# Kernel optimization log

Measured on AMD Instinct MI355X. Metric: run time of the kernel, lower is better.

## Reference

```python
import jax, jax.numpy as jnp
import numpy as np

B, S, D, H, DFF = 8, 1024, 1024, 16, 4096
DK = D // H
NEG = -1000000000.0


def layernorm(x, g, b, eps=1e-5):
    mu = jnp.mean(x, axis=-1, keepdims=True)
    var = jnp.mean((x - mu) ** 2, axis=-1, keepdims=True)
    return (x - mu) / jnp.sqrt(var + eps) * g + b


def setup_inputs() -> dict:
    key = jax.random.key(0)
    ks = jax.random.split(key, 16)
    s = 0.02
    inp = {
        "x": jax.random.normal(ks[0], (B, S, D), jnp.float32),
        "binary_mask": jax.random.randint(ks[1], (B, S), 0, 2, jnp.int32),
        # per-head projections stacked: [H, D, DK]
        "Wq": jax.random.normal(ks[2], (H, D, DK), jnp.float32) * s,
        "bq": jnp.zeros((H, DK), jnp.float32),
        "Wk": jax.random.normal(ks[3], (H, D, DK), jnp.float32) * s,
        "bk": jnp.zeros((H, DK), jnp.float32),
        "Wv": jax.random.normal(ks[4], (H, D, DK), jnp.float32) * s,
        "bv": jnp.zeros((H, DK), jnp.float32),
        "Wo": jax.random.normal(ks[5], (D, D), jnp.float32) * s,
        "bo": jnp.zeros((D,), jnp.float32),
        "ga": jnp.ones((D,), jnp.float32),
        "ba": jnp.zeros((D,), jnp.float32),
        "W1": jax.random.normal(ks[6], (D, DFF), jnp.float32) * s,
        "b1": jnp.zeros((DFF,), jnp.float32),
        "W2": jax.random.normal(ks[7], (DFF, D), jnp.float32) * s,
        "b2": jnp.zeros((D,), jnp.float32),
        "gf": jnp.ones((D,), jnp.float32),
        "bf": jnp.zeros((D,), jnp.float32),
    }
    return inp


def encoder_fwd(x, binary_mask, Wq, bq, Wk, bk, Wv, bv, Wo, bo, ga, ba, W1, b1, W2, b2, gf, bf):
    # --- multi-head self-attention (heads vectorized over h axis) ---
    q = jnp.einsum("bsd,hdk->bhsk", x, Wq) + bq[None, :, None, :]
    k = jnp.einsum("bsd,hdk->bhsk", x, Wk) + bk[None, :, None, :]
    v = jnp.einsum("bsd,hdk->bhsk", x, Wv) + bv[None, :, None, :]
    score = jnp.einsum("bhik,bhjk->bhij", q, k) / jnp.sqrt(jnp.float32(DK))
    # mask: binary_mask is over KEY positions, broadcast over query dim
    score = score + jnp.where(binary_mask[:, None, None, :] == 0, NEG, 0.0)
    # NOTE: original code softmaxes over dim=1 of [B,Sq,Sk] -> the QUERY axis
    probs = jax.nn.softmax(score, axis=2)
    ctx = jnp.einsum("bhij,bhjk->bhik", probs, v)  # [B,H,S,DK]
    ctx = jnp.transpose(ctx, (0, 2, 1, 3)).reshape(x.shape[0], x.shape[1], D)
    attn_out = ctx @ Wo + bo
    y = layernorm(x + attn_out, ga, ba)
    # --- FFN ---
    h = jax.nn.relu(y @ W1 + b1)
    ffn_out = h @ W2 + b2
    return layernorm(y + ffn_out, gf, bf)


def reference(x, binary_mask, Wq, bq, Wk, bk, Wv, bv, Wo, bo, ga, ba, W1, b1, W2, b2, gf, bf):
    return encoder_fwd(x, binary_mask, Wq, bq, Wk, bk, Wv, bv, Wo, bo, ga, ba, W1, b1, W2, b2, gf, bf)
```

## Files before the change

kernel.cpp:

```cpp
#include <hip/hip_runtime.h>
#include <hip/hip_bf16.h>

typedef __bf16 bf16;
typedef __bf16 bf16x8 __attribute__((ext_vector_type(8)));
typedef __bf16 bf16x4 __attribute__((ext_vector_type(4)));
typedef float  f32x4  __attribute__((ext_vector_type(4)));

#define NB 8
#define NS 1024
#define ND 1024
#define NH 16
#define NDK 64
#define NDFF 4096

static __device__ __forceinline__ f32x4 mfma16(bf16x8 a, bf16x8 b, f32x4 c) {
    return __builtin_amdgcn_mfma_f32_16x16x32_bf16(a, b, c, 0, 0, 0);
}

#define GLDS(g, l) __builtin_amdgcn_global_load_lds( \
    (const __attribute__((address_space(1))) void*)(g), \
    (__attribute__((address_space(3))) void*)(l), 16, 0, 0)

__global__ __launch_bounds__(256) void cvt_x(const float* __restrict__ in,
                                             bf16* __restrict__ out, int n4)
{
    int idx = blockIdx.x * 256 + threadIdx.x;
    if (idx >= n4) return;
    float4 v = ((const float4*)in)[idx];
    bf16x4 o = { (bf16)v.x, (bf16)v.y, (bf16)v.z, (bf16)v.w };
    ((bf16x4*)out)[idx] = o;
}

__global__ __launch_bounds__(256) void prep_transpose(
    const float* __restrict__ Wq, const float* __restrict__ Wk, const float* __restrict__ Wv,
    const float* __restrict__ Wo, const float* __restrict__ W1, const float* __restrict__ W2,
    bf16* __restrict__ wqkvT, bf16* __restrict__ WoT,
    bf16* __restrict__ W1T, bf16* __restrict__ W2T)
{
    __shared__ float T[64][65];
    int bid = blockIdx.x;
    const float* src; bf16* dst; int srcLd, dstLd, tR, tC; bool scale = false;
    if (bid < 768) {
        int mat = bid >> 4, ty = bid & 15;
        int h = mat & 15, type = mat >> 4;
        const float* W = (type == 0) ? Wq : (type == 1 ? Wk : Wv);
        src = W + (size_t)h * ND * NDK;
        srcLd = NDK; tR = ty * 64; tC = 0;
        dst = wqkvT + ((size_t)type * 1024 + h * 64) * ND;
        dstLd = ND;
        scale = (type == 0);
    } else if (bid < 1024) {
        int b2 = bid - 768; int ty = b2 >> 4, tx = b2 & 15;
        src = Wo; srcLd = ND; tR = ty * 64; tC = tx * 64; dst = WoT; dstLd = ND;
    } else if (bid < 2048) {
        int b2 = bid - 1024; int ty = b2 >> 6, tx = b2 & 63;
        src = W1; srcLd = NDFF; tR = ty * 64; tC = tx * 64; dst = W1T; dstLd = ND;
    } else {
        int b2 = bid - 2048; int ty = b2 >> 4, tx = b2 & 15;
        src = W2; srcLd = ND; tR = ty * 64; tC = tx * 64; dst = W2T; dstLd = NDFF;
    }
    int t = threadIdx.x;
    int c0 = t & 63, r0 = t >> 6;
    #pragma unroll
    for (int rr = 0; rr < 16; rr++) {
        int row = rr * 4 + r0;
        T[row][c0] = src[(size_t)(tR + row) * srcLd + tC + c0];
    }
    __syncthreads();
    #pragma unroll
    for (int cc = 0; cc < 16; cc++) {
        int col = cc * 4 + r0;
        float v = T[c0][col];
        if (scale) v *= 0.125f;
        dst[(size_t)(tC + col) * dstLd + tR + c0] = (bf16)v;
    }
}

__global__ void prep_bias(const float* __restrict__ bq, const float* __restrict__ bk,
                          const float* __restrict__ bv, float* __restrict__ bqkv)
{
    int n = blockIdx.x * 256 + threadIdx.x;
    if (n >= 3072) return;
    int type = n >> 10, hk = n & 1023;
    const float* bb = (type == 0) ? bq : (type == 1 ? bk : bv);
    float v = bb[hk];
    if (type == 0) v *= 0.125f;
    bqkv[n] = v;
}

__global__ __launch_bounds__(256) void mask_scan(const int* __restrict__ mask,
                                                 int* __restrict__ newpos,
                                                 int* __restrict__ Ucnt)
{
    int b = blockIdx.x, t = threadIdx.x;
    __shared__ int sums[256];
    __shared__ int scans[257];
    const int* mb = mask + b * NS;
    int m[4], s = 0;
    #pragma unroll
    for (int k = 0; k < 4; k++) { m[k] = (mb[t * 4 + k] != 0) ? 1 : 0; s += m[k]; }
    sums[t] = s;
    __syncthreads();
    if (t == 0) {
        int acc = 0;
        for (int i = 0; i < 256; i++) { scans[i] = acc; acc += sums[i]; }
        scans[256] = acc;
        Ucnt[b] = acc;
    }
    __syncthreads();
    int U = scans[256];
    int p = scans[t];
    #pragma unroll
    for (int k = 0; k < 4; k++) {
        int j = t * 4 + k;
        newpos[b * NS + j] = m[k] ? p : U + (j - p);
        p += m[k];
    }
}

__global__ __launch_bounds__(256) void cvec_kernel(const bf16* __restrict__ Vb,
                                                   const int* __restrict__ Ucnt,
                                                   float* __restrict__ cvec)
{
    int bh = blockIdx.x, b = bh >> 4;
    int U = Ucnt[b];
    int t = threadIdx.x, kk = t & 63, ss = t >> 6;
    const bf16* Vp = Vb + (size_t)bh * NS * NDK;
    float a = 0.f;
    for (int s = U + ss; s < NS; s += 4) a += (float)Vp[s * NDK + kk];
    __shared__ float red[4][64];
    red[ss][kk] = a;
    __syncthreads();
    if (ss == 0)
        cvec[bh * 64 + kk] = (red[0][kk] + red[1][kk] + red[2][kk] + red[3][kk]) * (1.f / 1024.f);
}

__device__ __forceinline__ void gemm_bt_core(
    const bf16* __restrict__ A, const bf16* __restrict__ BT, int K,
    int rowBase, int colBase, f32x4 (&acc)[4][4], bf16* As, bf16* Bs)
{
    const int tid = threadIdx.x;
    const int lane = tid & 63, wid = tid >> 6;
    const int wr = (wid >> 1) * 64, wc = (wid & 1) * 64;
    const int lrow = lane & 15, lq = lane >> 4;
    const int srow = wid * 32 + (lane >> 3);
    const int gblk = (lane & 7) ^ ((lane >> 3) & 7);
    const bf16* Arow = A + (size_t)(rowBase + srow) * K + gblk * 8;
    const bf16* Brow = BT + (size_t)(colBase + srow) * K + gblk * 8;
    const int co0 = ((lq) ^ (lrow & 7)) * 8;
    const int co1 = ((4 + lq) ^ (lrow & 7)) * 8;
    f32x4 zz = {0.f, 0.f, 0.f, 0.f};
    #pragma unroll
    for (int i = 0; i < 4; i++)
        #pragma unroll
        for (int j = 0; j < 4; j++) acc[i][j] = zz;
    for (int k0 = 0; k0 < K; k0 += 64) {
        __syncthreads();
        #pragma unroll
        for (int it = 0; it < 4; it++)
            GLDS(Arow + (size_t)it * 8 * K + k0, As + (wid * 32 + it * 8) * 64);
        #pragma unroll
        for (int it = 0; it < 4; it++)
            GLDS(Brow + (size_t)it * 8 * K + k0, Bs + (wid * 32 + it * 8) * 64);
        __syncthreads();
        #pragma unroll
        for (int kh = 0; kh < 2; kh++) {
            const int co = kh ? co1 : co0;
            bf16x8 af[4], bfr[4];
            #pragma unroll
            for (int tt = 0; tt < 4; tt++) {
                af[tt]  = *(const bf16x8*)&As[(wr + tt * 16 + lrow) * 64 + co];
                bfr[tt] = *(const bf16x8*)&Bs[(wc + tt * 16 + lrow) * 64 + co];
            }
            #pragma unroll
            for (int i = 0; i < 4; i++)
                #pragma unroll
                for (int j = 0; j < 4; j++)
                    acc[i][j] = mfma16(af[i], bfr[j], acc[i][j]);
        }
    }
}

__device__ __forceinline__ void gemm8p(
    const bf16* __restrict__ A, const bf16* __restrict__ BT, int K,
    int rowBase, int colBase, f32x4 (&acc)[8][4], bf16* As, bf16* Bs)
{
    constexpr int SETSZ = 256 * 64;
    const int tid = threadIdx.x, lane = tid & 63, wid = tid >> 6;
    const int wm = wid >> 2, wn = wid & 3;
    const int lrow = lane & 15, lq = lane >> 4;
    const int s8 = lane >> 3, gblk = (lane & 7) ^ s8;
    const int co0 = (lq ^ (lrow & 7)) * 8;
    const int co1 = ((4 + lq) ^ (lrow & 7)) * 8;
    f32x4 zz = {0.f, 0.f, 0.f, 0.f};
    #pragma unroll
    for (int i = 0; i < 8; i++)
        #pragma unroll
        for (int j = 0; j < 4; j++) acc[i][j] = zz;
    const bf16* Ag = A  + (size_t)(rowBase + wid * 8 + s8) * K + gblk * 8;
    const bf16* Bg = BT + (size_t)(colBase + wid * 8 + s8) * K + gblk * 8;

#define SG_A(kt, set, h) do { \
    GLDS(Ag + (size_t)((h) * 128) * K + (kt) * 64, \
         As + (set) * SETSZ + ((h) * 128 + wid * 8) * 64); \
    GLDS(Ag + (size_t)((h) * 128 + 64) * K + (kt) * 64, \
         As + (set) * SETSZ + ((h) * 128 + 64 + wid * 8) * 64); \
} while (0)
#define SG_B(kt, set, h) do { \
    GLDS(Bg + (size_t)((h) * 128) * K + (kt) * 64, \
         Bs + (set) * SETSZ + ((h) * 128 + wid * 8) * 64); \
    GLDS(Bg + (size_t)((h) * 128 + 64) * K + (kt) * 64, \
         Bs + (set) * SETSZ + ((h) * 128 + 64 + wid * 8) * 64); \
} while (0)
#define RD_A(dst, base, ms) do { _Pragma("unroll") for (int i_ = 0; i_ < 4; i_++) { \
    int ro_ = (wm * 128 + (ms) * 64 + i_ * 16 + lrow) * 64; \
    dst[i_][0] = *(const bf16x8*)&(base)[ro_ + co0]; \
    dst[i_][1] = *(const bf16x8*)&(base)[ro_ + co1]; } } while (0)
#define RD_B(dst, base, ns) do { _Pragma("unroll") for (int j_ = 0; j_ < 2; j_++) { \
    int ro_ = (wn * 64 + (ns) * 32 + j_ * 16 + lrow) * 64; \
    dst[j_][0] = *(const bf16x8*)&(base)[ro_ + co0]; \
    dst[j_][1] = *(const bf16x8*)&(base)[ro_ + co1]; } } while (0)
#define CL8(av, bv, ms, ns) do { \
    __builtin_amdgcn_s_setprio(1); \
    _Pragma("unroll") for (int i_ = 0; i_ < 4; i_++) \
    _Pragma("unroll") for (int j_ = 0; j_ < 2; j_++) { \
        acc[(ms) * 4 + i_][(ns) * 2 + j_] = \
            mfma16(av[i_][0], bv[j_][0], acc[(ms) * 4 + i_][(ns) * 2 + j_]); \
        acc[(ms) * 4 + i_][(ns) * 2 + j_] = \
            mfma16(av[i_][1], bv[j_][1], acc[(ms) * 4 + i_][(ns) * 2 + j_]); } \
    __builtin_amdgcn_s_setprio(0); \
} while (0)
#define BAR8 __builtin_amdgcn_s_barrier()
#define VM4 asm volatile("s_waitcnt vmcnt(4)" ::: "memory")
#define VM0 asm volatile("s_waitcnt vmcnt(0)" ::: "memory")

    const int nt = K >> 6, nIter = nt >> 1;
    SG_B(0, 0, 0); SG_B(0, 0, 1);
    SG_A(0, 0, 0); SG_A(0, 0, 1);
    SG_B(1, 1, 0); SG_B(1, 1, 1);
    VM4; BAR8;
    const bf16* A0b = As;           const bf16* B0b = Bs;
    const bf16* A1b = As + SETSZ;   const bf16* B1b = Bs + SETSZ;
    for (int J = 0; J < nIter; ++J) {
        const int v = 2 * J + 1;
        const bool pf = (J + 1 < nIter);
        bf16x8 a0[4][2], a1[4][2], b0[2][2], b1[2][2];
        RD_A(a0, A0b, 0); RD_B(b0, B0b, 0);
        SG_A(v, 1, 0);
        BAR8; CL8(a0, b0, 0, 0); BAR8;
        RD_B(b1, B0b, 1);
        SG_A(v, 1, 1);
        BAR8; CL8(a0, b1, 0, 1); BAR8;
        RD_A(a1, A0b, 1);
        if (pf) SG_B(v + 1, 0, 0);
        BAR8; CL8(a1, b1, 1, 1); BAR8;
        if (pf) SG_B(v + 1, 0, 1);
        BAR8; CL8(a1, b0, 1, 0);
        if (pf) { VM4; } else { VM0; }
        BAR8;
        RD_A(a0, A1b, 0); RD_B(b0, B1b, 0);
        if (pf) SG_A(v + 1, 0, 0);
        BAR8; CL8(a0, b0, 0, 0); BAR8;
        RD_B(b1, B1b, 1);
        if (pf) SG_A(v + 1, 0, 1);
        BAR8; CL8(a0, b1, 0, 1); BAR8;
        RD_A(a1, A1b, 1);
        if (pf) SG_B(v + 2, 1, 0);
        BAR8; CL8(a1, b1, 1, 1); BAR8;
        if (pf) SG_B(v + 2, 1, 1);
        BAR8; CL8(a1, b0, 1, 0);
        if (pf) { VM4; } else { VM0; }
        BAR8;
    }
#undef SG_A
#undef SG_B
#undef RD_A
#undef RD_B
#undef CL8
#undef BAR8
#undef VM4
#undef VM0
}

__device__ __forceinline__ void gemmB_core(
    const bf16* __restrict__ A, const bf16* __restrict__ BT, int K,
    int rowBase, int colBase, f32x4 (&acc)[4][4], bf16* As, bf16* Bs)
{
    constexpr int ABUF = 128 * 64, BBUF = 256 * 64;
    const int tid = threadIdx.x, lane = tid & 63, wid = tid >> 6;
    const int wm = wid >> 2, wn = wid & 3;
    const int lrow = lane & 15, lq = lane >> 4;
    const int srow = lane >> 3, gblk = (lane & 7) ^ srow;
    const int co0 = (lq ^ (lrow & 7)) * 8;
    const int co1 = ((4 + lq) ^ (lrow & 7)) * 8;
    f32x4 zz = {0.f, 0.f, 0.f, 0.f};
    #pragma unroll
    for (int i = 0; i < 4; i++)
        #pragma unroll
        for (int j = 0; j < 4; j++) acc[i][j] = zz;
    const bf16* Ag = A  + (size_t)(rowBase + wid * 8 + srow) * K + gblk * 8;
    const bf16* Bg = BT + (size_t)(colBase + wid * 8 + srow) * K + gblk * 8;

#define SGA2(kt, bi, rr) GLDS(Ag + (size_t)(kt) * 64 + (size_t)(rr) * 64 * K, \
                              As + (bi) * ABUF + ((rr) * 64 + wid * 8) * 64)
#define SGB2(kt, bi, rr) GLDS(Bg + (size_t)(kt) * 64 + (size_t)(rr) * 64 * K, \
                              Bs + (bi) * BBUF + ((rr) * 64 + wid * 8) * 64)
#define RDA2() do { _Pragma("unroll") for (int i_ = 0; i_ < 4; i_++) { \
    int ro_ = (wm * 64 + i_ * 16 + lrow) * 64; \
    af[i_][0] = *(const bf16x8*)&Ab[ro_ + co0]; \
    af[i_][1] = *(const bf16x8*)&Ab[ro_ + co1]; } } while (0)
#define RDB2(dst, NS_) do { _Pragma("unroll") for (int j_ = 0; j_ < 2; j_++) { \
    int ro_ = (wn * 64 + (NS_) * 32 + j_ * 16 + lrow) * 64; \
    dst[j_][0] = *(const bf16x8*)&Bb[ro_ + co0]; \
    dst[j_][1] = *(const bf16x8*)&Bb[ro_ + co1]; } } while (0)
#define CLUSTER_B(bfx, JO) do { \
    __builtin_amdgcn_s_barrier(); \
    asm volatile("s_waitcnt lgkmcnt(0)" ::: "memory"); \
    __builtin_amdgcn_sched_barrier(0); \
    __builtin_amdgcn_s_setprio(1); \
    _Pragma("unroll") \
    for (int i_ = 0; i_ < 4; i_++) \
        _Pragma("unroll") \
        for (int j_ = 0; j_ < 2; j_++) { \
            acc[i_][(JO) + j_] = mfma16(af[i_][0], bfx[j_][0], acc[i_][(JO) + j_]); \
            acc[i_][(JO) + j_] = mfma16(af[i_][1], bfx[j_][1], acc[i_][(JO) + j_]); \
        } \
    __builtin_amdgcn_s_setprio(0); \
} while (0)

    const int nt = K >> 6;
    SGA2(0, 0, 0); SGA2(0, 0, 1);
    SGB2(0, 0, 0); SGB2(0, 0, 1); SGB2(0, 0, 2); SGB2(0, 0, 3);
    SGA2(1, 1, 0); SGA2(1, 1, 1);
    SGB2(1, 1, 0); SGB2(1, 1, 1); SGB2(1, 1, 2); SGB2(1, 1, 3);
    asm volatile("s_waitcnt vmcnt(6)" ::: "memory");
    __builtin_amdgcn_s_barrier();

    int ci = 0, si = 2;
    for (int t = 0; t < nt; ++t) {
        const bf16* Ab = As + ci * ABUF;
        const bf16* Bb = Bs + ci * BBUF;
        const bool pf = (t + 2 < nt);
        bf16x8 af[4][2], bf0[2][2], bf1[2][2];
        RDA2(); RDB2(bf0, 0);
        if (pf) { SGA2(t + 2, si, 0); SGA2(t + 2, si, 1); SGB2(t + 2, si, 0); SGB2(t + 2, si, 1); }
        CLUSTER_B(bf0, 0);
        __builtin_amdgcn_s_barrier();
        RDB2(bf1, 1);
        if (pf) { SGB2(t + 2, si, 2); SGB2(t + 2, si, 3); }
        CLUSTER_B(bf1, 2);
        if (pf)                asm volatile("s_waitcnt vmcnt(6)" ::: "memory");
        else if (t + 1 < nt)   asm volatile("s_waitcnt vmcnt(0)" ::: "memory");
        __builtin_amdgcn_s_barrier();
        ci = (ci == 2) ? 0 : ci + 1;
        si = (si == 2) ? 0 : si + 1;
    }
#undef SGA2
#undef SGB2
#undef RDA2
#undef RDB2
#undef CLUSTER_B
}

__global__ __launch_bounds__(256) void g1_qkv(
    const bf16* __restrict__ x, const bf16* __restrict__ wqkvT, const float* __restrict__ bqkv,
    const int* __restrict__ newpos,
    bf16* __restrict__ Q, bf16* __restrict__ Kb, bf16* __restrict__ Vb)
{
    __shared__ bf16 As[128 * 64], Bs[128 * 64];
    f32x4 acc[4][4];
    int rowBase = blockIdx.x * 128, colBase = blockIdx.y * 128;
    gemm_bt_core(x, wqkvT, ND, rowBase, colBase, acc, As, Bs);
    const int tid = threadIdx.x, lane = tid & 63, wid = tid >> 6;
    const int wr = (wid >> 1) * 64, wc = (wid & 1) * 64, lrow = lane & 15, lq = lane >> 4;
    const int type = colBase >> 10;
    int spv[4][4];
    if (type != 0) {
        #pragma unroll
        for (int i = 0; i < 4; i++)
            #pragma unroll
            for (int r = 0; r < 4; r++) {
                int grow = rowBase + wr + i * 16 + lq * 4 + r;
                spv[i][r] = newpos[grow];
            }
    }
    #pragma unroll
    for (int j = 0; j < 4; j++) {
        int gcol = colBase + wc + j * 16 + lrow;
        float bias = bqkv[gcol];
        int h = (gcol >> 6) & 15, kk = gcol & 63;
        bf16* dst = (type == 0) ? Q : (type == 1 ? Kb : Vb);
        #pragma unroll
        for (int i = 0; i < 4; i++) {
            #pragma unroll
            for (int r = 0; r < 4; r++) {
                int grow = rowBase + wr + i * 16 + lq * 4 + r;
                int b = grow >> 10;
                int s = (type == 0) ? (grow & 1023) : spv[i][r];
                dst[((size_t)(b * NH + h) * NS + s) * NDK + kk] = (bf16)(acc[i][j][r] + bias);
            }
        }
    }
}

__global__ __launch_bounds__(256) void vt_trans(
    const bf16* __restrict__ Vb, bf16* __restrict__ Vt)
{
    __shared__ bf16 T[64 * 72];
    int bh = blockIdx.y, s0 = blockIdx.x * 64;
    const bf16* src = Vb + ((size_t)bh * NS + s0) * NDK;
    int tid = threadIdx.x;
    #pragma unroll
    for (int it = 0; it < 2; it++) {
        int g = tid + it * 256;
        int row = g >> 3, c = (g & 7) * 8;
        *(bf16x8*)&T[row * 72 + c] = *(const bf16x8*)&src[row * NDK + c];
    }
    __syncthreads();
    #pragma unroll
    for (int it = 0; it < 2; it++) {
        int g = tid + it * 256;
        int kk = g >> 3, sc = (g & 7) * 8;
        bf16x8 v;
        #pragma unroll
        for (int t = 0; t < 8; t++) v[t] = T[(sc + t) * 72 + kk];
        *(bf16x8*)&Vt[((size_t)bh * NDK + kk) * NS + s0 + sc] = v;
    }
}

__global__ __launch_bounds__(256) void g2_stats(
    const bf16* __restrict__ Q, const bf16* __restrict__ Kb,
    const int* __restrict__ Ucnt, float2* __restrict__ alpha)
{
    __shared__ bf16 Qs[128 * 64];
    int bh = blockIdx.y, b = bh >> 4;
    int jBase = blockIdx.x * 128;
    int U = Ucnt[b];
    const int tid = threadIdx.x;
    if (jBase >= U) {
        if (tid < 128) {
            float2 z; z.x = 0.f; z.y = 0.f;
            alpha[(size_t)bh * NS + jBase + tid] = z;
        }
        return;
    }
    const bf16* Kp = Kb + (size_t)bh * NS * NDK;
    const bf16* Qp = Q + (size_t)bh * NS * NDK;
    const int lane = tid & 63, wid = tid >> 6;
    const int lrow = lane & 15, lq = lane >> 4;
    bf16x8 kf[2][2];
    #pragma unroll
    for (int jt = 0; jt < 2; jt++)
        #pragma unroll
        for (int kh = 0; kh < 2; kh++)
            kf[jt][kh] = *(const bf16x8*)&Kp[(size_t)(jBase + wid * 32 + jt * 16 + lrow) * NDK + kh * 32 + lq * 8];
    const int srow = lane >> 3;
    const int gblk = (lane & 7) ^ srow;
    float Lacc[2][4];
    #pragma unroll
    for (int jt = 0; jt < 2; jt++)
        #pragma unroll
        for (int r = 0; r < 4; r++) Lacc[jt][r] = 0.f;
    f32x4 zz = {0.f, 0.f, 0.f, 0.f};
    for (int i0 = 0; i0 < NS; i0 += 128) {
        __syncthreads();
        #pragma unroll
        for (int it = 0; it < 4; it++)
            GLDS(Qp + (size_t)(i0 + wid * 32 + it * 8 + srow) * NDK + gblk * 8,
                 Qs + (wid * 32 + it * 8) * 64);
        __syncthreads();
        #pragma unroll
        for (int it = 0; it < 8; it++) {
            bf16x8 qb[2];
            #pragma unroll
            for (int kh = 0; kh < 2; kh++)
                qb[kh] = *(const bf16x8*)&Qs[(it * 16 + lrow) * 64 + ((kh * 4 + lq) ^ (lrow & 7)) * 8];
            #pragma unroll
            for (int jt = 0; jt < 2; jt++) {
                f32x4 s = mfma16(kf[jt][0], qb[0], zz);
                s = mfma16(kf[jt][1], qb[1], s);
                #pragma unroll
                for (int r = 0; r < 4; r++) Lacc[jt][r] += __expf(s[r]);
            }
        }
    }
    #pragma unroll
    for (int jt = 0; jt < 2; jt++) {
        #pragma unroll
        for (int r = 0; r < 4; r++) {
            float v = Lacc[jt][r];
            v += __shfl_xor(v, 1); v += __shfl_xor(v, 2);
            v += __shfl_xor(v, 4); v += __shfl_xor(v, 8);
            if (lrow == 0) {
                int j = jBase + wid * 32 + jt * 16 + lq * 4 + r;
                float2 ac;
                ac.x = (j < U) ? 1.f / v : 0.f;
                ac.y = 0.f;
                alpha[(size_t)bh * NS + j] = ac;
            }
        }
    }
}

__global__ __launch_bounds__(256) void g3_ctx(
    const bf16* __restrict__ Q, const bf16* __restrict__ Kb, const bf16* __restrict__ Vt,
    const float2* __restrict__ alpha, const int* __restrict__ Ucnt,
    const float* __restrict__ cvec, bf16* __restrict__ ctx)
{
    __shared__ bf16 Ks[64 * 64];
    __shared__ bf16 Vs[64 * 64];
    __shared__ bf16 Ps[4 * 64 * 64];
    int bh = blockIdx.y, iBase = blockIdx.x * 256;
    int b = bh >> 4, h = bh & 15;
    int U = Ucnt[b];
    int Ur = (U + 63) & ~63;
    const bf16* Qp = Q + (size_t)bh * NS * NDK;
    const bf16* Kp = Kb + (size_t)bh * NS * NDK;
    const bf16* Vp = Vt + (size_t)bh * NDK * NS;
    const float2* al = alpha + (size_t)bh * NS;
    const int tid = threadIdx.x, lane = tid & 63, wid = tid >> 6;
    const int lrow = lane & 15, lq = lane >> 4;
    const int iw = iBase + wid * 64;
    bf16x8 qf[4][2];
    #pragma unroll
    for (int it = 0; it < 4; it++)
        #pragma unroll
        for (int kh = 0; kh < 2; kh++)
            qf[it][kh] = *(const bf16x8*)&Qp[(size_t)(iw + it * 16 + lrow) * NDK + kh * 32 + lq * 8];
    const int srow = lane >> 3;
    const int gblk = (lane & 7) ^ srow;
    f32x4 cacc[4][4];
    f32x4 zz = {0.f, 0.f, 0.f, 0.f};
    #pragma unroll
    for (int it = 0; it < 4; it++)
        #pragma unroll
        for (int kt = 0; kt < 4; kt++) cacc[it][kt] = zz;
    bf16* Pw = Ps + wid * 64 * 64;
    for (int j0 = 0; j0 < Ur; j0 += 64) {
        __syncthreads();
        #pragma unroll
        for (int it = 0; it < 2; it++)
            GLDS(Kp + (size_t)(j0 + wid * 16 + it * 8 + srow) * NDK + gblk * 8,
                 Ks + (wid * 16 + it * 8) * 64);
        #pragma unroll
        for (int it = 0; it < 2; it++)
            GLDS(Vp + (size_t)(wid * 16 + it * 8 + srow) * NS + j0 + gblk * 8,
                 Vs + (wid * 16 + it * 8) * 64);
        __syncthreads();
        bf16x8 kb[4][2];
        #pragma unroll
        for (int jt = 0; jt < 4; jt++)
            #pragma unroll
            for (int kh = 0; kh < 2; kh++)
                kb[jt][kh] = *(const bf16x8*)&Ks[(jt * 16 + lrow) * 64 + ((kh * 4 + lq) ^ (lrow & 7)) * 8];
        #pragma unroll
        for (int jt = 0; jt < 4; jt++) {
            float2 acj[4];
            #pragma unroll
            for (int r = 0; r < 4; r++) acj[r] = al[j0 + jt * 16 + lq * 4 + r];
            #pragma unroll
            for (int it = 0; it < 4; it++) {
                f32x4 s = mfma16(kb[jt][0], qf[it][0], zz);
                s = mfma16(kb[jt][1], qf[it][1], s);
                bf16x4 pv;
                #pragma unroll
                for (int r = 0; r < 4; r++)
                    pv[r] = (bf16)(acj[r].x * __expf(s[r]) + acj[r].y);
                int i = it * 16 + lrow;
                int jb = jt * 2 + (lq >> 1);
                *(bf16x4*)&Pw[i * 64 + ((jb ^ (i & 7)) * 8) + (lq & 1) * 4] = pv;
            }
        }
        bf16x8 vb[4][2];
        #pragma unroll
        for (int kt = 0; kt < 4; kt++)
            #pragma unroll
            for (int kh = 0; kh < 2; kh++)
                vb[kt][kh] = *(const bf16x8*)&Vs[(kt * 16 + lrow) * 64 + ((kh * 4 + lq) ^ (lrow & 7)) * 8];
        #pragma unroll
        for (int it = 0; it < 4; it++) {
            bf16x8 pa[2];
            #pragma unroll
            for (int kh = 0; kh < 2; kh++)
                pa[kh] = *(const bf16x8*)&Pw[(it * 16 + lrow) * 64 + ((kh * 4 + lq) ^ (lrow & 7)) * 8];
            #pragma unroll
            for (int kt = 0; kt < 4; kt++) {
                cacc[it][kt] = mfma16(pa[0], vb[kt][0], cacc[it][kt]);
                cacc[it][kt] = mfma16(pa[1], vb[kt][1], cacc[it][kt]);
            }
        }
    }
    #pragma unroll
    for (int kt = 0; kt < 4; kt++) {
        int col = h * NDK + kt * 16 + lrow;
        float cv = cvec[bh * 64 + kt * 16 + lrow];
        #pragma unroll
        for (int it = 0; it < 4; it++) {
            #pragma unroll
            for (int r = 0; r < 4; r++) {
                int i = iw + it * 16 + lq * 4 + r;
                ctx[(size_t)(b * NS + i) * ND + col] = (bf16)(cacc[it][kt][r] + cv);
            }
        }
    }
}

__global__ __launch_bounds__(256) void g4_proj(
    const bf16* __restrict__ ctx, const bf16* __restrict__ WoT, const float* __restrict__ bo,
    const bf16* __restrict__ xb, bf16* __restrict__ t1b)
{
    __shared__ bf16 As[128 * 64], Bs[128 * 64];
    f32x4 acc[4][4];
    int rowBase = blockIdx.x * 128, colBase = blockIdx.y * 128;
    gemm_bt_core(ctx, WoT, ND, rowBase, colBase, acc, As, Bs);
    const int tid = threadIdx.x, lane = tid & 63, wid = tid >> 6;
    const int wr = (wid >> 1) * 64, wc = (wid & 1) * 64, lrow = lane & 15, lq = lane >> 4;
    #pragma unroll
    for (int j = 0; j < 4; j++) {
        int gcol = colBase + wc + j * 16 + lrow;
        float bias = bo[gcol];
        #pragma unroll
        for (int i = 0; i < 4; i++) {
            #pragma unroll
            for (int r = 0; r < 4; r++) {
                int grow = rowBase + wr + i * 16 + lq * 4 + r;
                float v = acc[i][j][r] + bias + (float)xb[(size_t)grow * ND + gcol];
                t1b[(size_t)grow * ND + gcol] = (bf16)v;
            }
        }
    }
}

__global__ __launch_bounds__(512, 2) void g5_ffn1(
    const bf16* __restrict__ y, const bf16* __restrict__ W1T, const float* __restrict__ b1,
    bf16* __restrict__ hb)
{
    __shared__ bf16 As[2 * 256 * 64], Bs[2 * 256 * 64];
    f32x4 acc[8][4];
    int g = blockIdx.x;
    int sw = (g & 7) * 64 + (g >> 3);
    int bm = sw >> 4, bn = sw & 15;
    int rowBase = bm * 256, colBase = bn * 256;
    gemm8p(y, W1T, ND, rowBase, colBase, acc, As, Bs);
    const int tid = threadIdx.x, lane = tid & 63, wid = tid >> 6;
    const int wm = wid >> 2, wn = wid & 3, lrow = lane & 15, lq = lane >> 4;
    #pragma unroll
    for (int j = 0; j < 4; j++) {
        int gcol = colBase + wn * 64 + j * 16 + lrow;
        float bias = b1[gcol];
        #pragma unroll
        for (int i = 0; i < 8; i++) {
            #pragma unroll
            for (int r = 0; r < 4; r++) {
                int grow = rowBase + wm * 128 + i * 16 + lq * 4 + r;
                float v = fmaxf(acc[i][j][r] + bias, 0.f);
                hb[(size_t)grow * NDFF + gcol] = (bf16)v;
            }
        }
    }
}

__global__ __launch_bounds__(512, 2) void g6_ffn2(
    const bf16* __restrict__ hb, const bf16* __restrict__ W2T, const float* __restrict__ b2,
    const bf16* __restrict__ yb, bf16* __restrict__ zb)
{
    __shared__ bf16 As[3 * 128 * 64], Bs[3 * 256 * 64];
    f32x4 acc[4][4];
    int g = blockIdx.x;
    int sw = (g & 7) * 32 + (g >> 3);
    int bm = sw >> 2, bn = sw & 3;
    int rowBase = bm * 128, colBase = bn * 256;
    gemmB_core(hb, W2T, NDFF, rowBase, colBase, acc, As, Bs);
    const int tid = threadIdx.x, lane = tid & 63, wid = tid >> 6;
    const int wm = wid >> 2, wn = wid & 3, lrow = lane & 15, lq = lane >> 4;
    #pragma unroll
    for (int j = 0; j < 4; j++) {
        int gcol = colBase + wn * 64 + j * 16 + lrow;
        float bias = b2[gcol];
        #pragma unroll
        for (int i = 0; i < 4; i++) {
            #pragma unroll
            for (int r = 0; r < 4; r++) {
                int grow = rowBase + wm * 64 + i * 16 + lq * 4 + r;
                float v = acc[i][j][r] + bias + (float)yb[(size_t)grow * ND + gcol];
                zb[(size_t)grow * ND + gcol] = (bf16)v;
            }
        }
    }
}

__global__ __launch_bounds__(256) void ln_kernel(
    const bf16* __restrict__ in, bf16* __restrict__ outb, float* __restrict__ outf,
    const float* __restrict__ g, const float* __restrict__ bb)
{
    int row = blockIdx.x, tid = threadIdx.x;
    const bf16* p = in + (size_t)row * ND;
    bf16x4 v4 = *(const bf16x4*)&p[tid * 4];
    float vv[4] = {(float)v4[0], (float)v4[1], (float)v4[2], (float)v4[3]};
    float s = vv[0] + vv[1] + vv[2] + vv[3];
    float q = vv[0]*vv[0] + vv[1]*vv[1] + vv[2]*vv[2] + vv[3]*vv[3];
    #pragma unroll
    for (int m = 1; m < 64; m <<= 1) { s += __shfl_xor(s, m); q += __shfl_xor(q, m); }
    __shared__ float rs[4], rq[4];
    int wid = tid >> 6, lane = tid & 63;
    if (lane == 0) { rs[wid] = s; rq[wid] = q; }
    __syncthreads();
    s = rs[0] + rs[1] + rs[2] + rs[3];
    q = rq[0] + rq[1] + rq[2] + rq[3];
    float mean = s * (1.f / 1024.f);
    float var = q * (1.f / 1024.f) - mean * mean;
    float rstd = 1.f / sqrtf(var + 1e-5f);
    float4 of;
    bf16x4 ob;
    #pragma unroll
    for (int k = 0; k < 4; k++) {
        int col = tid * 4 + k;
        float yv = (vv[k] - mean) * rstd * g[col] + bb[col];
        ((float*)&of)[k] = yv;
        ob[k] = (bf16)yv;
    }
    if (outb) *(bf16x4*)&outb[(size_t)row * ND + tid * 4] = ob;
    if (outf) ((float4*)(outf + (size_t)row * ND))[tid] = of;
}

extern "C" void kernel_launch(void* const* d_in, const int* in_sizes, int n_in,
                              void* d_out, int out_size, void* d_ws, size_t ws_size,
                              hipStream_t stream)
{
    const float* x    = (const float*)d_in[0];
    const int*   mask = (const int*)d_in[1];
    const float* Wq   = (const float*)d_in[2];
    const float* bq   = (const float*)d_in[3];
    const float* Wk   = (const float*)d_in[4];
    const float* bk   = (const float*)d_in[5];
    const float* Wv   = (const float*)d_in[6];
    const float* bv   = (const float*)d_in[7];
    const float* Wo   = (const float*)d_in[8];
    const float* bo   = (const float*)d_in[9];
    const float* ga   = (const float*)d_in[10];
    const float* ba   = (const float*)d_in[11];
    const float* W1   = (const float*)d_in[12];
    const float* b1   = (const float*)d_in[13];
    const float* W2   = (const float*)d_in[14];
    const float* b2   = (const float*)d_in[15];
    const float* gf   = (const float*)d_in[16];
    const float* bfb  = (const float*)d_in[17];

    size_t off = 0;
    auto alloc = [&](size_t n) { char* p = (char*)d_ws + off; off += (n + 255) & ~(size_t)255; return (void*)p; };
    bf16*   wqkvT = (bf16*)  alloc((size_t)3072 * 1024 * 2);
    bf16*   WoT   = (bf16*)  alloc((size_t)1024 * 1024 * 2);
    bf16*   W1T   = (bf16*)  alloc((size_t)4096 * 1024 * 2);
    bf16*   W2T   = (bf16*)  alloc((size_t)1024 * 4096 * 2);
    float*  bqkv  = (float*) alloc(3072 * 4);
    float2* alpha = (float2*)alloc((size_t)NB * NH * NS * 8);
    int*    newpos= (int*)   alloc((size_t)NB * NS * 4);
    int*    Ucnt  = (int*)   alloc(NB * 4);
    float*  cvec  = (float*) alloc((size_t)NB * NH * NDK * 4);
    bf16*   xb    = (bf16*)  alloc((size_t)8192 * 1024 * 2);
    bf16*   ub    = (bf16*)  alloc((size_t)8192 * 4096 * 2);
    bf16*   Qb    = ub;
    bf16*   Kb    = ub + (size_t)8192 * 1024;
    bf16*   Vt    = ub + (size_t)2 * 8192 * 1024;
    bf16*   ctx   = ub + (size_t)3 * 8192 * 1024;
    bf16*   hb    = ub;
    bf16*   t1b   = (bf16*)  alloc((size_t)8192 * 1024 * 2);
    bf16*   Vb    = t1b;
    bf16*   zb    = t1b;
    bf16*   yb    = (bf16*)  alloc((size_t)8192 * 1024 * 2);

    cvt_x<<<8192, 256, 0, stream>>>(x, xb, 8192 * 1024 / 4);
    prep_transpose<<<3072, 256, 0, stream>>>(Wq, Wk, Wv, Wo, W1, W2, wqkvT, WoT, W1T, W2T);
    prep_bias<<<12, 256, 0, stream>>>(bq, bk, bv, bqkv);
    mask_scan<<<8, 256, 0, stream>>>(mask, newpos, Ucnt);
    g1_qkv<<<dim3(64, 24), 256, 0, stream>>>(xb, wqkvT, bqkv, newpos, Qb, Kb, Vb);
    vt_trans<<<dim3(16, 128), 256, 0, stream>>>(Vb, Vt);
    cvec_kernel<<<128, 256, 0, stream>>>(Vb, Ucnt, cvec);
    g2_stats<<<dim3(8, 128), 256, 0, stream>>>(Qb, Kb, Ucnt, alpha);
    g3_ctx<<<dim3(4, 128), 256, 0, stream>>>(Qb, Kb, Vt, alpha, Ucnt, cvec, ctx);
    g4_proj<<<dim3(64, 8), 256, 0, stream>>>(ctx, WoT, bo, xb, t1b);
    ln_kernel<<<8192, 256, 0, stream>>>(t1b, yb, nullptr, ga, ba);
    g5_ffn1<<<512, 512, 0, stream>>>(yb, W1T, b1, hb);
    g6_ffn2<<<256, 512, 0, stream>>>(hb, W2T, b2, yb, zb);
    ln_kernel<<<8192, 256, 0, stream>>>(zb, nullptr, (float*)d_out, gf, bfb);
}
```

Measured before the change: 507.8 us.

## Merge prep kernels, move QKV GEMM to larger tile core, fuse cvec into V transpose

Result: faster. 472.8 us (-6.9%).

```diff
diff --git a/kernel.cpp b/kernel.cpp
--- a/kernel.cpp
+++ b/kernel.cpp
@@ -21,118 +21,97 @@
     (const __attribute__((address_space(1))) void*)(g), \
     (__attribute__((address_space(3))) void*)(l), 16, 0, 0)
 
-__global__ __launch_bounds__(256) void cvt_x(const float* __restrict__ in,
-                                             bf16* __restrict__ out, int n4)
-{
-    int idx = blockIdx.x * 256 + threadIdx.x;
-    if (idx >= n4) return;
-    float4 v = ((const float4*)in)[idx];
-    bf16x4 o = { (bf16)v.x, (bf16)v.y, (bf16)v.z, (bf16)v.w };
-    ((bf16x4*)out)[idx] = o;
-}
-
-__global__ __launch_bounds__(256) void prep_transpose(
+__global__ __launch_bounds__(256) void prep_all(
+    const float* __restrict__ x, const int* __restrict__ mask,
     const float* __restrict__ Wq, const float* __restrict__ Wk, const float* __restrict__ Wv,
     const float* __restrict__ Wo, const float* __restrict__ W1, const float* __restrict__ W2,
-    bf16* __restrict__ wqkvT, bf16* __restrict__ WoT,
-    bf16* __restrict__ W1T, bf16* __restrict__ W2T)
-{
-    __shared__ float T[64][65];
-    int bid = blockIdx.x;
-    const float* src; bf16* dst; int srcLd, dstLd, tR, tC; bool scale = false;
-    if (bid < 768) {
-        int mat = bid >> 4, ty = bid & 15;
-        int h = mat & 15, type = mat >> 4;
-        const float* W = (type == 0) ? Wq : (type == 1 ? Wk : Wv);
-        src = W + (size_t)h * ND * NDK;
-        srcLd = NDK; tR = ty * 64; tC = 0;
-        dst = wqkvT + ((size_t)type * 1024 + h * 64) * ND;
-        dstLd = ND;
-        scale = (type == 0);
-    } else if (bid < 1024) {
-        int b2 = bid - 768; int ty = b2 >> 4, tx = b2 & 15;
-        src = Wo; srcLd = ND; tR = ty * 64; tC = tx * 64; dst = WoT; dstLd = ND;
-    } else if (bid < 2048) {
-        int b2 = bid - 1024; int ty = b2 >> 6, tx = b2 & 63;
-        src = W1; srcLd = NDFF; tR = ty * 64; tC = tx * 64; dst = W1T; dstLd = ND;
+    const float* __restrict__ bq, const float* __restrict__ bk, const float* __restrict__ bv,
+    bf16* __restrict__ xb, bf16* __restrict__ wqkvT, bf16* __restrict__ WoT,
+    bf16* __restrict__ W1T, bf16* __restrict__ W2T, float* __restrict__ bqkv,
+    int* __restrict__ newpos, int* __restrict__ Ucnt, float* __restrict__ cvec)
+{
+    __shared__ __align__(16) char shraw[64 * 65 * 4];
+    int bid = blockIdx.x, t = threadIdx.x;
+    if (bid < 8192) {
+        int idx = bid * 256 + t;
+        float4 v = ((const float4*)x)[idx];
+        bf16x4 o = { (bf16)v.x, (bf16)v.y, (bf16)v.z, (bf16)v.w };
+        ((bf16x4*)xb)[idx] = o;
+    } else if (bid < 11264) {
+        float (*T)[65] = (float (*)[65])shraw;
+        int tb = bid - 8192;
+        const float* src; bf16* dst; int srcLd, dstLd, tR, tC; bool scale = false;
+        if (tb < 768) {
+            int mat = tb >> 4, ty = tb & 15;
+            int h = mat & 15, type = mat >> 4;
+            const float* W = (type == 0) ? Wq : (type == 1 ? Wk : Wv);
+            src = W + (size_t)h * ND * NDK;
+            srcLd = NDK; tR = ty * 64; tC = 0;
+            dst = wqkvT + ((size_t)type * 1024 + h * 64) * ND;
+            dstLd = ND;
+            scale = (type == 0);
+        } else if (tb < 1024) {
+            int b2 = tb - 768; int ty = b2 >> 4, tx = b2 & 15;
+            src = Wo; srcLd = ND; tR = ty * 64; tC = tx * 64; dst = WoT; dstLd = ND;
+        } else if (tb < 2048) {
+            int b2 = tb - 1024; int ty = b2 >> 6, tx = b2 & 63;
+            src = W1; srcLd = NDFF; tR = ty * 64; tC = tx * 64; dst = W1T; dstLd = ND;
+        } else {
+            int b2 = tb - 2048; int ty = b2 >> 4, tx = b2 & 15;
+            src = W2; srcLd = ND; tR = ty * 64; tC = tx * 64; dst = W2T; dstLd = NDFF;
+        }
+        int c0 = t & 63, r0 = t >> 6;
+        #pragma unroll
+        for (int rr = 0; rr < 16; rr++) {
+            int row = rr * 4 + r0;
+            T[row][c0] = src[(size_t)(tR + row) * srcLd + tC + c0];
+        }
+        __syncthreads();
+        #pragma unroll
+        for (int cc = 0; cc < 16; cc++) {
+            int col = cc * 4 + r0;
+            float v = T[c0][col];
+            if (scale) v *= 0.125f;
+            dst[(size_t)(tC + col) * dstLd + tR + c0] = (bf16)v;
+        }
+    } else if (bid < 11276) {
+        int n = (bid - 11264) * 256 + t;
+        if (n < 3072) {
+            int type = n >> 10, hk = n & 1023;
+            const float* bb = (type == 0) ? bq : (type == 1 ? bk : bv);
+            float v = bb[hk];
+            if (type == 0) v *= 0.125f;
+            bqkv[n] = v;
+        }
+    } else if (bid < 11284) {
+        int* sums  = (int*)shraw;
+        int* scans = (int*)(shraw + 1024);
+        int b = bid - 11276;
+        const int* mb = mask + b * NS;
+        int m[4], s = 0;
+        #pragma unroll
+        for (int k = 0; k < 4; k++) { m[k] = (mb[t * 4 + k] != 0) ? 1 : 0; s += m[k]; }
+        sums[t] = s;
+        __syncthreads();
+        if (t == 0) {
+            int acc = 0;
+            for (int i = 0; i < 256; i++) { scans[i] = acc; acc += sums[i]; }
+            scans[256] = acc;
+            Ucnt[b] = acc;
+        }
+        __syncthreads();
+        int U = scans[256];
+        int p = scans[t];
+        #pragma unroll
+        for (int k = 0; k < 4; k++) {
+            int j = t * 4 + k;
+            newpos[b * NS + j] = m[k] ? p : U + (j - p);
+            p += m[k];
+        }
     } else {
-        int b2 = bid - 2048; int ty = b2 >> 4, tx = b2 & 15;
-        src = W2; srcLd = ND; tR = ty * 64; tC = tx * 64; dst = W2T; dstLd = NDFF;
-    }
-    int t = threadIdx.x;
-    int c0 = t & 63, r0 = t >> 6;
-    #pragma unroll
-    for (int rr = 0; rr < 16; rr++) {
-        int row = rr * 4 + r0;
-        T[row][c0] = src[(size_t)(tR + row) * srcLd + tC + c0];
-    }
-    __syncthreads();
-    #pragma unroll
-    for (int cc = 0; cc < 16; cc++) {
-        int col = cc * 4 + r0;
-        float v = T[c0][col];
-        if (scale) v *= 0.125f;
-        dst[(size_t)(tC + col) * dstLd + tR + c0] = (bf16)v;
-    }
-}
-
-__global__ void prep_bias(const float* __restrict__ bq, const float* __restrict__ bk,
-                          const float* __restrict__ bv, float* __restrict__ bqkv)
-{
-    int n = blockIdx.x * 256 + threadIdx.x;
-    if (n >= 3072) return;
-    int type = n >> 10, hk = n & 1023;
-    const float* bb = (type == 0) ? bq : (type == 1 ? bk : bv);
-    float v = bb[hk];
-    if (type == 0) v *= 0.125f;
-    bqkv[n] = v;
-}
-
-__global__ __launch_bounds__(256) void mask_scan(const int* __restrict__ mask,
-                                                 int* __restrict__ newpos,
-                                                 int* __restrict__ Ucnt)
-{
-    int b = blockIdx.x, t = threadIdx.x;
-    __shared__ int sums[256];
-    __shared__ int scans[257];
-    const int* mb = mask + b * NS;
-    int m[4], s = 0;
-    #pragma unroll
-    for (int k = 0; k < 4; k++) { m[k] = (mb[t * 4 + k] != 0) ? 1 : 0; s += m[k]; }
-    sums[t] = s;
-    __syncthreads();
-    if (t == 0) {
-        int acc = 0;
-        for (int i = 0; i < 256; i++) { scans[i] = acc; acc += sums[i]; }
-        scans[256] = acc;
-        Ucnt[b] = acc;
-    }
-    __syncthreads();
-    int U = scans[256];
-    int p = scans[t];
-    #pragma unroll
-    for (int k = 0; k < 4; k++) {
-        int j = t * 4 + k;
-        newpos[b * NS + j] = m[k] ? p : U + (j - p);
-        p += m[k];
-    }
-}
-
-__global__ __launch_bounds__(256) void cvec_kernel(const bf16* __restrict__ Vb,
-                                                   const int* __restrict__ Ucnt,
-                                                   float* __restrict__ cvec)
-{
-    int bh = blockIdx.x, b = bh >> 4;
-    int U = Ucnt[b];
-    int t = threadIdx.x, kk = t & 63, ss = t >> 6;
-    const bf16* Vp = Vb + (size_t)bh * NS * NDK;
-    float a = 0.f;
-    for (int s = U + ss; s < NS; s += 4) a += (float)Vp[s * NDK + kk];
-    __shared__ float red[4][64];
-    red[ss][kk] = a;
-    __syncthreads();
-    if (ss == 0)
-        cvec[bh * 64 + kk] = (red[0][kk] + red[1][kk] + red[2][kk] + red[3][kk]) * (1.f / 1024.f);
+        float4 z = {0.f, 0.f, 0.f, 0.f};
+        ((float4*)cvec)[(bid - 11284) * 256 + t] = z;
+    }
 }
 
 __device__ __forceinline__ void gemm_bt_core(
@@ -362,17 +341,20 @@
 #undef CLUSTER_B
 }
 
-__global__ __launch_bounds__(256) void g1_qkv(
+__global__ __launch_bounds__(512, 2) void g1_qkv(
     const bf16* __restrict__ x, const bf16* __restrict__ wqkvT, const float* __restrict__ bqkv,
     const int* __restrict__ newpos,
     bf16* __restrict__ Q, bf16* __restrict__ Kb, bf16* __restrict__ Vb)
 {
-    __shared__ bf16 As[128 * 64], Bs[128 * 64];
+    __shared__ bf16 As[3 * 128 * 64], Bs[3 * 256 * 64];
     f32x4 acc[4][4];
-    int rowBase = blockIdx.x * 128, colBase = blockIdx.y * 128;
-    gemm_bt_core(x, wqkvT, ND, rowBase, colBase, acc, As, Bs);
+    int g = blockIdx.x;
+    int sw = (g & 7) * 96 + (g >> 3);
+    int bm = sw / 12, bn = sw % 12;
+    int rowBase = bm * 128, colBase = bn * 256;
+    gemmB_core(x, wqkvT, ND, rowBase, colBase, acc, As, Bs);
     const int tid = threadIdx.x, lane = tid & 63, wid = tid >> 6;
-    const int wr = (wid >> 1) * 64, wc = (wid & 1) * 64, lrow = lane & 15, lq = lane >> 4;
+    const int wm = wid >> 2, wn = wid & 3, lrow = lane & 15, lq = lane >> 4;
     const int type = colBase >> 10;
     int spv[4][4];
     if (type != 0) {
@@ -380,13 +362,13 @@
         for (int i = 0; i < 4; i++)
             #pragma unroll
             for (int r = 0; r < 4; r++) {
-                int grow = rowBase + wr + i * 16 + lq * 4 + r;
+                int grow = rowBase + wm * 64 + i * 16 + lq * 4 + r;
                 spv[i][r] = newpos[grow];
             }
     }
     #pragma unroll
     for (int j = 0; j < 4; j++) {
-        int gcol = colBase + wc + j * 16 + lrow;
+        int gcol = colBase + wn * 64 + j * 16 + lrow;
         float bias = bqkv[gcol];
         int h = (gcol >> 6) & 15, kk = gcol & 63;
         bf16* dst = (type == 0) ? Q : (type == 1 ? Kb : Vb);
@@ -394,7 +376,7 @@
         for (int i = 0; i < 4; i++) {
             #pragma unroll
             for (int r = 0; r < 4; r++) {
-                int grow = rowBase + wr + i * 16 + lq * 4 + r;
+                int grow = rowBase + wm * 64 + i * 16 + lq * 4 + r;
                 int b = grow >> 10;
                 int s = (type == 0) ? (grow & 1023) : spv[i][r];
                 dst[((size_t)(b * NH + h) * NS + s) * NDK + kk] = (bf16)(acc[i][j][r] + bias);
@@ -404,9 +386,11 @@
 }
 
 __global__ __launch_bounds__(256) void vt_trans(
-    const bf16* __restrict__ Vb, bf16* __restrict__ Vt)
+    const bf16* __restrict__ Vb, const int* __restrict__ Ucnt,
+    bf16* __restrict__ Vt, float* __restrict__ cvec)
 {
     __shared__ bf16 T[64 * 72];
+    __shared__ float red[4][64];
     int bh = blockIdx.y, s0 = blockIdx.x * 64;
     const bf16* src = Vb + ((size_t)bh * NS + s0) * NDK;
     int tid = threadIdx.x;
@@ -425,6 +409,18 @@
         #pragma unroll
         for (int t = 0; t < 8; t++) v[t] = T[(sc + t) * 72 + kk];
         *(bf16x8*)&Vt[((size_t)bh * NDK + kk) * NS + s0 + sc] = v;
+    }
+    int U = Ucnt[bh >> 4];
+    int lo = U - s0;
+    if (lo < 0) lo = 0;
+    if (lo < 64) {
+        int kk = tid & 63, ss = tid >> 6;
+        float a = 0.f;
+        for (int r = lo + ss; r < 64; r += 4) a += (float)T[r * 72 + kk];
+        red[ss][kk] = a;
+        __syncthreads();
+        if (ss == 0)
+            atomicAdd(&cvec[bh * 64 + kk], red[0][kk] + red[1][kk] + red[2][kk] + red[3][kk]);
     }
 }
 
@@ -593,7 +589,7 @@
     #pragma unroll
     for (int kt = 0; kt < 4; kt++) {
         int col = h * NDK + kt * 16 + lrow;
-        float cv = cvec[bh * 64 + kt * 16 + lrow];
+        float cv = cvec[bh * 64 + kt * 16 + lrow] * (1.f / 1024.f);
         #pragma unroll
         for (int it = 0; it < 4; it++) {
             #pragma unroll
@@ -769,13 +765,10 @@
     bf16*   zb    = t1b;
     bf16*   yb    = (bf16*)  alloc((size_t)8192 * 1024 * 2);
 
-    cvt_x<<<8192, 256, 0, stream>>>(x, xb, 8192 * 1024 / 4);
-    prep_transpose<<<3072, 256, 0, stream>>>(Wq, Wk, Wv, Wo, W1, W2, wqkvT, WoT, W1T, W2T);
-    prep_bias<<<12, 256, 0, stream>>>(bq, bk, bv, bqkv);
-    mask_scan<<<8, 256, 0, stream>>>(mask, newpos, Ucnt);
-    g1_qkv<<<dim3(64, 24), 256, 0, stream>>>(xb, wqkvT, bqkv, newpos, Qb, Kb, Vb);
-    vt_trans<<<dim3(16, 128), 256, 0, stream>>>(Vb, Vt);
-    cvec_kernel<<<128, 256, 0, stream>>>(Vb, Ucnt, cvec);
+    prep_all<<<11292, 256, 0, stream>>>(x, mask, Wq, Wk, Wv, Wo, W1, W2, bq, bk, bv,
+                                        xb, wqkvT, WoT, W1T, W2T, bqkv, newpos, Ucnt, cvec);
+    g1_qkv<<<768, 512, 0, stream>>>(xb, wqkvT, bqkv, newpos, Qb, Kb, Vb);
+    vt_trans<<<dim3(16, 128), 256, 0, stream>>>(Vb, Ucnt, Vt, cvec);
     g2_stats<<<dim3(8, 128), 256, 0, stream>>>(Qb, Kb, Ucnt, alpha);
     g3_ctx<<<dim3(4, 128), 256, 0, stream>>>(Qb, Kb, Vt, alpha, Ucnt, cvec, ctx);
     g4_proj<<<dim3(64, 8), 256, 0, stream>>>(ctx, WoT, bo, xb, t1b);
```
